# Kernel optimization log

Measured on AMD Instinct MI355X. Metric: run time of the kernel, lower is better.

## Reference

```python
import jax, jax.numpy as jnp
import numpy as np

BLOCK = 32      # block_size
KB = 128        # K // BLOCK (mask rows)
NB = 128        # N // BLOCK (mask cols)
DENSITY = 0.1


def _make_mask_indices():
    rng = np.random.RandomState(0)
    mask = rng.rand(KB, NB) < DENSITY
    # guarantee no fully-empty output column (kernel writes zeros there anyway,
    # segment_sum also yields zeros, so this is only to keep stats sane)
    ii, jj = np.nonzero(mask)   # row-major order == torch.nonzero(mask)
    return ii.astype(np.int32), jj.astype(np.int32)


def setup_inputs() -> dict:
    key = jax.random.key(0)
    k1, k2 = jax.random.split(key)
    ii, jj = _make_mask_indices()
    nnz = ii.shape[0]
    M = 4096
    K = KB * BLOCK
    x = jax.random.normal(k1, (M, K), dtype=jnp.float32)
    # block-sparse weight: one [BLOCK, BLOCK] tile per nonzero mask entry,
    # stored in row-major nonzero order (matches torch.nonzero ordering)
    w = jax.random.normal(k2, (nnz, BLOCK, BLOCK), dtype=jnp.float32) * 0.02
    return {"x": x, "w": w, "idx_i": jnp.asarray(ii), "idx_j": jnp.asarray(jj)}


def reference(x, w, idx_i, idx_j):
    # y[:, j*B:(j+1)*B] += x[:, i*B:(i+1)*B] @ w[blk] for each nonzero block (i, j)
    M, K = x.shape
    nnz, B, _ = w.shape
    xb = x.reshape(M, K // B, B)[:, idx_i, :]                 # [M, nnz, B] gather
    partial = jnp.einsum('mnk,nkj->nmj', xb, w)               # [nnz, M, B]
    yb = jax.ops.segment_sum(partial, idx_j, num_segments=NB)  # [NB, M, B] scatter-add
    return yb.transpose(1, 0, 2).reshape(M, NB * B)           # [M, N]
```

## Files before the change

kernel.cpp:

```cpp
#include <hip/hip_runtime.h>
#include <hip/hip_bf16.h>

typedef __bf16 bf16x8 __attribute__((ext_vector_type(8)));
typedef __bf16 bf16x4 __attribute__((ext_vector_type(4)));
typedef float f32x4 __attribute__((ext_vector_type(4)));

#define KDIM 4096
#define NDIM 4096
#define NBJ  128
#define KB   128

#define NB      7
#define BLK_LDS 2560

__global__ __launch_bounds__(256) void k_prep(
    const float* __restrict__ x, const float* __restrict__ w,
    const int* __restrict__ idx_i, const int* __restrict__ idx_j,
    __bf16* __restrict__ xb, __bf16* __restrict__ wT,
    int* __restrict__ colptr, int* __restrict__ colinfo,
    int nnz, int M, int nbCvt) {
    __shared__ char smem[2176];
    int b = blockIdx.x, t = threadIdx.x;

    if (b < nbCvt) {
        int i, m0;
        if ((M & 1023) == 0) {
            int cpx = M >> 9;
            int s = b & 7, r = b >> 3;
            int wch = r >> 7;
            i  = r & (KB - 1);
            m0 = (s * cpx + wch) * 64;
        } else {
            i  = b & (KB - 1);
            m0 = (b >> 7) * 64;
        }
        int q  = t & 3, r = t >> 2;
        const float* xp = x + (size_t)(m0 + r) * KDIM + i * 32 + q * 8;
        float4 u = ((const float4*)xp)[0];
        float4 v = ((const float4*)xp)[1];
        bf16x8 o;
        o[0]=(__bf16)u.x; o[1]=(__bf16)u.y; o[2]=(__bf16)u.z; o[3]=(__bf16)u.w;
        o[4]=(__bf16)v.x; o[5]=(__bf16)v.y; o[6]=(__bf16)v.z; o[7]=(__bf16)v.w;
        *(bf16x8*)(xb + ((size_t)i * M + m0 + r) * 32 + q * 8) = o;
    } else if (b < nbCvt + nnz) {
        auto tile = (__bf16(*)[33])smem;
        int n = b - nbCvt;
        float4 v = ((const float4*)(w + (size_t)n * 1024))[t];
        int e = t * 4, k = e >> 5, c = e & 31;
        tile[k][c + 0] = (__bf16)v.x; tile[k][c + 1] = (__bf16)v.y;
        tile[k][c + 2] = (__bf16)v.z; tile[k][c + 3] = (__bf16)v.w;
        __syncthreads();
        int f = t * 4, cc = f >> 5, kk = f & 31;
        bf16x4 o;
        o[0] = tile[kk + 0][cc]; o[1] = tile[kk + 1][cc];
        o[2] = tile[kk + 2][cc]; o[3] = tile[kk + 3][cc];
        ((bf16x4*)(wT + (size_t)n * 1024))[t] = o;
    } else {
        int* cnt = (int*)smem;
        int* cur = cnt + NBJ;
        if (t < NBJ) cnt[t] = 0;
        __syncthreads();
        for (int n = t; n < nnz; n += 256) atomicAdd(&cnt[idx_j[n]], 1);
        __syncthreads();
        int mycount = (t < NBJ) ? cnt[t] : 0;
        for (int off = 1; off < NBJ; off <<= 1) {
            int add = (t < NBJ && t >= off) ? cnt[t - off] : 0;
            __syncthreads();
            if (t < NBJ) cnt[t] += add;
            __syncthreads();
        }
        if (t < NBJ) {
            colptr[t + 1] = cnt[t];
            cur[t] = cnt[t] - mycount;
            if (t == 0) colptr[0] = 0;
        }
        __syncthreads();
        for (int n = t; n < nnz; n += 256) {
            int j = idx_j[n];
            int pos = atomicAdd(&cur[j], 1);
            colinfo[pos] = (idx_i[n] << 16) | n;
        }
    }
}

struct AFrag { bf16x8 a0, a1; };

#define MFMA4(A, B0, B1)                                                       \
    acc[0][0] = __builtin_amdgcn_mfma_f32_16x16x32_bf16(A.a0, B0, acc[0][0], 0, 0, 0); \
    acc[0][1] = __builtin_amdgcn_mfma_f32_16x16x32_bf16(A.a0, B1, acc[0][1], 0, 0, 0); \
    acc[1][0] = __builtin_amdgcn_mfma_f32_16x16x32_bf16(A.a1, B0, acc[1][0], 0, 0, 0); \
    acc[1][1] = __builtin_amdgcn_mfma_f32_16x16x32_bf16(A.a1, B1, acc[1][1], 0, 0, 0);

__global__ __launch_bounds__(256, 8) void k_bsmm(
    const __bf16* __restrict__ xb, const __bf16* __restrict__ wT,
    const int* __restrict__ colptr, const int* __restrict__ colinfo,
    float* __restrict__ y, int M) {
    __shared__ int nfo[64];
    __shared__ __attribute__((aligned(16))) char wbuf[NB * BLK_LDS];

    int RCH = M >> 7;
    int l = blockIdx.x;
    int rc, j;
    if ((RCH & 7) == 0) {
        int rps = RCH >> 3;
        int s = l & 7, u = l >> 3;
        rc = s * rps + (u >> 7);
        j  = u & (NBJ - 1);
    } else {
        rc = l % RCH; j = l / RCH;
    }
    int t = threadIdx.x;
    int lane = t & 63, wave = t >> 6;
    int quad = lane >> 4, l16 = lane & 15;
    int wrow = rc * 128 + wave * 32;

    int beg = colptr[j], end = colptr[j + 1];
    int cnt = end - beg;

    f32x4 acc[2][2] = {};

    size_t strideA = (size_t)M * 32;
    const __bf16* xbase = xb + (size_t)(wrow + l16) * 32 + quad * 8;
    const char*   wread = wbuf + l16 * 80 + quad * 16;

    if (cnt > 0 && cnt <= 64) {
        if (t < cnt) nfo[t] = colinfo[beg + t];
        __syncthreads();

        for (int bb0 = 0; bb0 < cnt; bb0 += NB) {
            int cb = cnt - bb0; if (cb > NB) cb = NB;
            if (bb0 > 0) __syncthreads();

            for (int c = t; c < cb * 128; c += 256) {
                int b = c >> 7, w16 = c & 127;
                int n = nfo[bb0 + b] & 0xFFFF;
                bf16x8 v = *(const bf16x8*)(wT + (size_t)n * 1024 + w16 * 8);
                *(bf16x8*)(wbuf + b * BLK_LDS + (w16 >> 2) * 80 + (w16 & 3) * 16) = v;
            }
            __syncthreads();

            auto fa = [&](int p) {
                int pp = p < cb ? p : cb - 1;
                int ib = nfo[bb0 + pp] >> 16;
                AFrag f;
                const __bf16* xp = xbase + (size_t)ib * strideA;
                f.a0 = *(const bf16x8*)(xp);
                f.a1 = *(const bf16x8*)(xp + 16 * 32);
                return f;
            };
            AFrag A0 = fa(0);
            AFrag A1 = fa(1);
            for (int p = 0; p < cb; ++p) {
                const char* wp = wread + p * BLK_LDS;
                bf16x8 b0 = *(const bf16x8*)(wp);
                bf16x8 b1 = *(const bf16x8*)(wp + 16 * 80);
                MFMA4(A0, b0, b1);
                A0 = A1; A1 = fa(p + 2);
            }
        }
    } else if (cnt > 64) {
        for (int bb = beg; bb < end; bb += NB) {
            int cb = end - bb; if (cb > NB) cb = NB;
            if (bb > beg) __syncthreads();
            if (t < cb) nfo[t] = colinfo[bb + t];
            __syncthreads();
            for (int c = t; c < cb * 128; c += 256) {
                int b = c >> 7, w16 = c & 127;
                int n = nfo[b] & 0xFFFF;
                bf16x8 v = *(const bf16x8*)(wT + (size_t)n * 1024 + w16 * 8);
                *(bf16x8*)(wbuf + b * BLK_LDS + (w16 >> 2) * 80 + (w16 & 3) * 16) = v;
            }
            __syncthreads();
            auto fa = [&](int p) {
                int pp = p < cb ? p : cb - 1;
                int ib = nfo[pp] >> 16;
                AFrag f;
                const __bf16* xp = xbase + (size_t)ib * strideA;
                f.a0 = *(const bf16x8*)(xp);
                f.a1 = *(const bf16x8*)(xp + 16 * 32);
                return f;
            };
            AFrag A0 = fa(0);
            AFrag A1 = fa(1);
            for (int p = 0; p < cb; ++p) {
                const char* wp = wread + p * BLK_LDS;
                bf16x8 b0 = *(const bf16x8*)(wp);
                bf16x8 b1 = *(const bf16x8*)(wp + 16 * 80);
                MFMA4(A0, b0, b1);
                A0 = A1; A1 = fa(p + 2);
            }
        }
    }

    #pragma unroll
    for (int r = 0; r < 2; ++r)
        #pragma unroll
        for (int ch = 0; ch < 2; ++ch)
            #pragma unroll
            for (int reg = 0; reg < 4; ++reg) {
                int row = wrow + r * 16 + quad * 4 + reg;
                int col = j * 32 + ch * 16 + l16;
                __builtin_nontemporal_store(acc[r][ch][reg],
                                            &y[(size_t)row * NDIM + col]);
            }
}

__global__ __launch_bounds__(256) void k_bsmm_nows(
    const float* __restrict__ x, const float* __restrict__ w,
    const int* __restrict__ idx_i, const int* __restrict__ idx_j,
    float* __restrict__ y, int nnz) {
    __shared__ int list[256];
    __shared__ int listn;
    __shared__ __bf16 tw[32][40];
    int j = blockIdx.y;
    int tid = threadIdx.x;
    int lane = tid & 63, wave = tid >> 6;
    int quad = lane >> 4, l16 = lane & 15;
    int wrow = blockIdx.x * 256 + wave * 64;

    if (tid == 0) listn = 0;
    __syncthreads();
    for (int n = tid; n < nnz; n += 256)
        if (idx_j[n] == j) { int p = atomicAdd(&listn, 1); list[p & 255] = n; }
    __syncthreads();
    int cnt = listn;

    f32x4 acc[4][2] = {};
    for (int p = 0; p < cnt; ++p) {
        int n = list[p];
        int ib = idx_i[n];
        {
            float4 v = ((const float4*)(w + (size_t)n * 1024))[tid];
            int e = tid * 4, k = e >> 5, c = e & 31;
            tw[c + 0][k] = (__bf16)v.x; tw[c + 1][k] = (__bf16)v.y;
            tw[c + 2][k] = (__bf16)v.z; tw[c + 3][k] = (__bf16)v.w;
        }
        __syncthreads();
        bf16x8 a[4];
        #pragma unroll
        for (int r = 0; r < 4; ++r) {
            const float* xp = x + (size_t)(wrow + r * 16 + l16) * KDIM + ib * 32 + quad * 8;
            float4 u = *(const float4*)(xp);
            float4 v = *(const float4*)(xp + 4);
            a[r][0] = (__bf16)u.x; a[r][1] = (__bf16)u.y; a[r][2] = (__bf16)u.z; a[r][3] = (__bf16)u.w;
            a[r][4] = (__bf16)v.x; a[r][5] = (__bf16)v.y; a[r][6] = (__bf16)v.z; a[r][7] = (__bf16)v.w;
        }
        bf16x8 b0 = *(const bf16x8*)&tw[l16][quad * 8];
        bf16x8 b1 = *(const bf16x8*)&tw[l16 + 16][quad * 8];
        #pragma unroll
        for (int r = 0; r < 4; ++r) {
            acc[r][0] = __builtin_amdgcn_mfma_f32_16x16x32_bf16(a[r], b0, acc[r][0], 0, 0, 0);
            acc[r][1] = __builtin_amdgcn_mfma_f32_16x16x32_bf16(a[r], b1, acc[r][1], 0, 0, 0);
        }
        __syncthreads();
    }

    #pragma unroll
    for (int r = 0; r < 4; ++r)
        #pragma unroll
        for (int ch = 0; ch < 2; ++ch)
            #pragma unroll
            for (int reg = 0; reg < 4; ++reg) {
                int row = wrow + r * 16 + quad * 4 + reg;
                int col = j * 32 + ch * 16 + l16;
                y[(size_t)row * NDIM + col] = acc[r][ch][reg];
            }
}

extern "C" void kernel_launch(void* const* d_in, const int* in_sizes, int n_in,
                              void* d_out, int out_size, void* d_ws, size_t ws_size,
                              hipStream_t stream) {
    const float* x     = (const float*)d_in[0];
    const float* w     = (const float*)d_in[1];
    const int*   idx_i = (const int*)d_in[2];
    const int*   idx_j = (const int*)d_in[3];
    float*       y     = (float*)d_out;

    int nnz = in_sizes[2];
    int M   = in_sizes[0] / KDIM;

    size_t xb_bytes = (size_t)M * KDIM * 2;
    size_t wt_bytes = (size_t)nnz * 1024 * 2;
    size_t need = xb_bytes + wt_bytes + (size_t)(NBJ + 2 + nnz) * 4;

    if (ws_size >= need && (M & 255) == 0 && nnz < 65536) {
        __bf16* xb      = (__bf16*)d_ws;
        __bf16* wT      = (__bf16*)((char*)d_ws + xb_bytes);
        int*    colptr  = (int*)((char*)d_ws + xb_bytes + wt_bytes);
        int*    colinfo = colptr + NBJ + 1;
        int nbCvt = KB * (M / 64);
        k_prep<<<nbCvt + nnz + 1, 256, 0, stream>>>(x, w, idx_i, idx_j,
                                                    xb, wT, colptr, colinfo,
                                                    nnz, M, nbCvt);
        k_bsmm<<<(M / 128) * NBJ, 256, 0, stream>>>(xb, wT, colptr, colinfo, y, M);
    } else {
        k_bsmm_nows<<<dim3(M / 256, NBJ), 256, 0, stream>>>(x, w, idx_i, idx_j, y, nnz);
    }
}
```

Before: 171.3 us.

## Stage A and W tiles into LDS via direct global-to-LDS loads

Replaces register-prefetched global reads of the x slab and the register-staged copy of weight tiles with global_load_lds transfers that write both A and B tiles directly into LDS, then feeds the MFMAs from LDS. The batch size drops to 6 blocks, LDS use grows to about 60 KB per workgroup, and the occupancy hint in launch bounds is removed. Nontemporal output stores become plain stores. The aim is to cut VGPR staging and global-load latency in the inner loop. The cost is much lower occupancy from the larger LDS footprint, no overlap between loading and compute within a batch, and possible LDS bank conflicts from the unpadded 64-byte row stride.

```diff
diff --git a/kernel.cpp b/kernel.cpp
--- a/kernel.cpp
+++ b/kernel.cpp
@@ -10,8 +10,15 @@
 #define NBJ  128
 #define KB   128
 
-#define NB      7
-#define BLK_LDS 2560
+#define NB    6
+#define A_BLK 8192
+#define B_BLK 2048
+
+__device__ __forceinline__ void gload16(const void* g, void* l) {
+    __builtin_amdgcn_global_load_lds(
+        (const __attribute__((address_space(1))) void*)g,
+        (__attribute__((address_space(3))) void*)l, 16, 0, 0);
+}
 
 __global__ __launch_bounds__(256) void k_prep(
     const float* __restrict__ x, const float* __restrict__ w,
@@ -83,20 +90,19 @@
     }
 }
 
-struct AFrag { bf16x8 a0, a1; };
-
-#define MFMA4(A, B0, B1)                                                       \
-    acc[0][0] = __builtin_amdgcn_mfma_f32_16x16x32_bf16(A.a0, B0, acc[0][0], 0, 0, 0); \
-    acc[0][1] = __builtin_amdgcn_mfma_f32_16x16x32_bf16(A.a0, B1, acc[0][1], 0, 0, 0); \
-    acc[1][0] = __builtin_amdgcn_mfma_f32_16x16x32_bf16(A.a1, B0, acc[1][0], 0, 0, 0); \
-    acc[1][1] = __builtin_amdgcn_mfma_f32_16x16x32_bf16(A.a1, B1, acc[1][1], 0, 0, 0);
-
-__global__ __launch_bounds__(256, 8) void k_bsmm(
+#define MFMA4(A0, A1, B0, B1)                                                  \
+    acc[0][0] = __builtin_amdgcn_mfma_f32_16x16x32_bf16(A0, B0, acc[0][0], 0, 0, 0); \
+    acc[0][1] = __builtin_amdgcn_mfma_f32_16x16x32_bf16(A0, B1, acc[0][1], 0, 0, 0); \
+    acc[1][0] = __builtin_amdgcn_mfma_f32_16x16x32_bf16(A1, B0, acc[1][0], 0, 0, 0); \
+    acc[1][1] = __builtin_amdgcn_mfma_f32_16x16x32_bf16(A1, B1, acc[1][1], 0, 0, 0);
+
+__global__ __launch_bounds__(256) void k_bsmm(
     const __bf16* __restrict__ xb, const __bf16* __restrict__ wT,
     const int* __restrict__ colptr, const int* __restrict__ colinfo,
     float* __restrict__ y, int M) {
     __shared__ int nfo[64];
-    __shared__ __attribute__((aligned(16))) char wbuf[NB * BLK_LDS];
+    __shared__ __attribute__((aligned(16))) char abuf[NB * A_BLK];
+    __shared__ __attribute__((aligned(16))) char bbuf[NB * B_BLK];
 
     int RCH = M >> 7;
     int l = blockIdx.x;
@@ -120,8 +126,9 @@
     f32x4 acc[2][2] = {};
 
     size_t strideA = (size_t)M * 32;
-    const __bf16* xbase = xb + (size_t)(wrow + l16) * 32 + quad * 8;
-    const char*   wread = wbuf + l16 * 80 + quad * 16;
+    const __bf16* xslab = xb + (size_t)(rc * 128) * 32;
+    const int aoff0 = (wave * 32 + l16) * 64 + quad * 16;
+    const int boff0 = l16 * 64 + quad * 16;
 
     if (cnt > 0 && cnt <= 64) {
         if (t < cnt) nfo[t] = colinfo[beg + t];
@@ -131,31 +138,28 @@
             int cb = cnt - bb0; if (cb > NB) cb = NB;
             if (bb0 > 0) __syncthreads();
 
+            for (int c = t; c < cb * 512; c += 256) {
+                int b = c >> 9, off = c & 511;
+                int ib = nfo[bb0 + b] >> 16;
+                gload16(xslab + (size_t)ib * strideA + off * 8,
+                        abuf + b * A_BLK + off * 16);
+            }
             for (int c = t; c < cb * 128; c += 256) {
-                int b = c >> 7, w16 = c & 127;
+                int b = c >> 7, off = c & 127;
                 int n = nfo[bb0 + b] & 0xFFFF;
-                bf16x8 v = *(const bf16x8*)(wT + (size_t)n * 1024 + w16 * 8);
-                *(bf16x8*)(wbuf + b * BLK_LDS + (w16 >> 2) * 80 + (w16 & 3) * 16) = v;
-            }
-            __syncthreads();
-
-            auto fa = [&](int p) {
-                int pp = p < cb ? p : cb - 1;
-                int ib = nfo[bb0 + pp] >> 16;
-                AFrag f;
-                const __bf16* xp = xbase + (size_t)ib * strideA;
-                f.a0 = *(const bf16x8*)(xp);
-                f.a1 = *(const bf16x8*)(xp + 16 * 32);
-                return f;
-            };
-            AFrag A0 = fa(0);
-            AFrag A1 = fa(1);
+                gload16(wT + (size_t)n * 1024 + off * 8,
+                        bbuf + b * B_BLK + off * 16);
+            }
+            __syncthreads();
+
             for (int p = 0; p < cb; ++p) {
-                const char* wp = wread + p * BLK_LDS;
-                bf16x8 b0 = *(const bf16x8*)(wp);
-                bf16x8 b1 = *(const bf16x8*)(wp + 16 * 80);
-                MFMA4(A0, b0, b1);
-                A0 = A1; A1 = fa(p + 2);
+                const char* ap = abuf + p * A_BLK + aoff0;
+                const char* bp = bbuf + p * B_BLK + boff0;
+                bf16x8 a0 = *(const bf16x8*)(ap);
+                bf16x8 a1 = *(const bf16x8*)(ap + 16 * 64);
+                bf16x8 b0 = *(const bf16x8*)(bp);
+                bf16x8 b1 = *(const bf16x8*)(bp + 16 * 64);
+                MFMA4(a0, a1, b0, b1);
             }
         }
     } else if (cnt > 64) {
@@ -164,30 +168,27 @@
             if (bb > beg) __syncthreads();
             if (t < cb) nfo[t] = colinfo[bb + t];
             __syncthreads();
+            for (int c = t; c < cb * 512; c += 256) {
+                int b = c >> 9, off = c & 511;
+                int ib = nfo[b] >> 16;
+                gload16(xslab + (size_t)ib * strideA + off * 8,
+                        abuf + b * A_BLK + off * 16);
+            }
             for (int c = t; c < cb * 128; c += 256) {
-                int b = c >> 7, w16 = c & 127;
+                int b = c >> 7, off = c & 127;
                 int n = nfo[b] & 0xFFFF;
-                bf16x8 v = *(const bf16x8*)(wT + (size_t)n * 1024 + w16 * 8);
-                *(bf16x8*)(wbuf + b * BLK_LDS + (w16 >> 2) * 80 + (w16 & 3) * 16) = v;
-            }
-            __syncthreads();
-            auto fa = [&](int p) {
-                int pp = p < cb ? p : cb - 1;
-                int ib = nfo[pp] >> 16;
-                AFrag f;
-                const __bf16* xp = xbase + (size_t)ib * strideA;
-                f.a0 = *(const bf16x8*)(xp);
-                f.a1 = *(const bf16x8*)(xp + 16 * 32);
-                return f;
-            };
-            AFrag A0 = fa(0);
-            AFrag A1 = fa(1);
+                gload16(wT + (size_t)n * 1024 + off * 8,
+                        bbuf + b * B_BLK + off * 16);
+            }
+            __syncthreads();
             for (int p = 0; p < cb; ++p) {
-                const char* wp = wread + p * BLK_LDS;
-                bf16x8 b0 = *(const bf16x8*)(wp);
-                bf16x8 b1 = *(const bf16x8*)(wp + 16 * 80);
-                MFMA4(A0, b0, b1);
-                A0 = A1; A1 = fa(p + 2);
+                const char* ap = abuf + p * A_BLK + aoff0;
+                const char* bp = bbuf + p * B_BLK + boff0;
+                bf16x8 a0 = *(const bf16x8*)(ap);
+                bf16x8 a1 = *(const bf16x8*)(ap + 16 * 64);
+                bf16x8 b0 = *(const bf16x8*)(bp);
+                bf16x8 b1 = *(const bf16x8*)(bp + 16 * 64);
+                MFMA4(a0, a1, b0, b1);
             }
         }
     }
@@ -200,8 +201,7 @@
             for (int reg = 0; reg < 4; ++reg) {
                 int row = wrow + r * 16 + quad * 4 + reg;
                 int col = j * 32 + ch * 16 + l16;
-                __builtin_nontemporal_store(acc[r][ch][reg],
-                                            &y[(size_t)row * NDIM + col]);
+                y[(size_t)row * NDIM + col] = acc[r][ch][reg];
             }
 }
 
```

Measured after the change: 182.4 us. +6.5%, slower.

## Fuse x fp32-to-bf16 conversion into the block-sparse matmul loads

Applied to the files above, without the earlier changes.

Removes the separate prep pass that converted all of x to a bf16 workspace copy. The matmul kernel now gathers fp32 rows of x directly and converts them to bf16 in registers before the MFMA. This saves the full conversion read/write pass and its workspace. In exchange, the repeated gathers of x move twice the bytes, since each column block rereads x in fp32. Occupancy hint lowered and output stores switched from nontemporal to regular.

```diff
diff --git a/kernel.cpp b/kernel.cpp
--- a/kernel.cpp
+++ b/kernel.cpp
@@ -14,37 +14,17 @@
 #define BLK_LDS 2560
 
 __global__ __launch_bounds__(256) void k_prep(
-    const float* __restrict__ x, const float* __restrict__ w,
+    const float* __restrict__ w,
     const int* __restrict__ idx_i, const int* __restrict__ idx_j,
-    __bf16* __restrict__ xb, __bf16* __restrict__ wT,
+    __bf16* __restrict__ wT,
     int* __restrict__ colptr, int* __restrict__ colinfo,
-    int nnz, int M, int nbCvt) {
+    int nnz) {
     __shared__ char smem[2176];
     int b = blockIdx.x, t = threadIdx.x;
 
-    if (b < nbCvt) {
-        int i, m0;
-        if ((M & 1023) == 0) {
-            int cpx = M >> 9;
-            int s = b & 7, r = b >> 3;
-            int wch = r >> 7;
-            i  = r & (KB - 1);
-            m0 = (s * cpx + wch) * 64;
-        } else {
-            i  = b & (KB - 1);
-            m0 = (b >> 7) * 64;
-        }
-        int q  = t & 3, r = t >> 2;
-        const float* xp = x + (size_t)(m0 + r) * KDIM + i * 32 + q * 8;
-        float4 u = ((const float4*)xp)[0];
-        float4 v = ((const float4*)xp)[1];
-        bf16x8 o;
-        o[0]=(__bf16)u.x; o[1]=(__bf16)u.y; o[2]=(__bf16)u.z; o[3]=(__bf16)u.w;
-        o[4]=(__bf16)v.x; o[5]=(__bf16)v.y; o[6]=(__bf16)v.z; o[7]=(__bf16)v.w;
-        *(bf16x8*)(xb + ((size_t)i * M + m0 + r) * 32 + q * 8) = o;
-    } else if (b < nbCvt + nnz) {
+    if (b < nnz) {
         auto tile = (__bf16(*)[33])smem;
-        int n = b - nbCvt;
+        int n = b;
         float4 v = ((const float4*)(w + (size_t)n * 1024))[t];
         int e = t * 4, k = e >> 5, c = e & 31;
         tile[k][c + 0] = (__bf16)v.x; tile[k][c + 1] = (__bf16)v.y;
@@ -83,16 +63,23 @@
     }
 }
 
-struct AFrag { bf16x8 a0, a1; };
-
-#define MFMA4(A, B0, B1)                                                       \
-    acc[0][0] = __builtin_amdgcn_mfma_f32_16x16x32_bf16(A.a0, B0, acc[0][0], 0, 0, 0); \
-    acc[0][1] = __builtin_amdgcn_mfma_f32_16x16x32_bf16(A.a0, B1, acc[0][1], 0, 0, 0); \
-    acc[1][0] = __builtin_amdgcn_mfma_f32_16x16x32_bf16(A.a1, B0, acc[1][0], 0, 0, 0); \
-    acc[1][1] = __builtin_amdgcn_mfma_f32_16x16x32_bf16(A.a1, B1, acc[1][1], 0, 0, 0);
-
-__global__ __launch_bounds__(256, 8) void k_bsmm(
-    const __bf16* __restrict__ xb, const __bf16* __restrict__ wT,
+struct FStage { float4 u0, v0, u1, v1; };
+
+__device__ __forceinline__ bf16x8 cvt8(float4 u, float4 v) {
+    bf16x8 o;
+    o[0]=(__bf16)u.x; o[1]=(__bf16)u.y; o[2]=(__bf16)u.z; o[3]=(__bf16)u.w;
+    o[4]=(__bf16)v.x; o[5]=(__bf16)v.y; o[6]=(__bf16)v.z; o[7]=(__bf16)v.w;
+    return o;
+}
+
+#define MFMA4(A0, A1, B0, B1)                                                  \
+    acc[0][0] = __builtin_amdgcn_mfma_f32_16x16x32_bf16(A0, B0, acc[0][0], 0, 0, 0); \
+    acc[0][1] = __builtin_amdgcn_mfma_f32_16x16x32_bf16(A0, B1, acc[0][1], 0, 0, 0); \
+    acc[1][0] = __builtin_amdgcn_mfma_f32_16x16x32_bf16(A1, B0, acc[1][0], 0, 0, 0); \
+    acc[1][1] = __builtin_amdgcn_mfma_f32_16x16x32_bf16(A1, B1, acc[1][1], 0, 0, 0);
+
+__global__ __launch_bounds__(256, 6) void k_bsmm(
+    const float* __restrict__ x, const __bf16* __restrict__ wT,
     const int* __restrict__ colptr, const int* __restrict__ colinfo,
     float* __restrict__ y, int M) {
     __shared__ int nfo[64];
@@ -119,9 +106,9 @@
 
     f32x4 acc[2][2] = {};
 
-    size_t strideA = (size_t)M * 32;
-    const __bf16* xbase = xb + (size_t)(wrow + l16) * 32 + quad * 8;
-    const char*   wread = wbuf + l16 * 80 + quad * 16;
+    const float* xr0 = x + (size_t)(wrow + l16) * KDIM + quad * 8;
+    const float* xr1 = xr0 + (size_t)16 * KDIM;
+    const char*  wread = wbuf + l16 * 80 + quad * 16;
 
     if (cnt > 0 && cnt <= 64) {
         if (t < cnt) nfo[t] = colinfo[beg + t];
@@ -139,23 +126,26 @@
             }
             __syncthreads();
 
-            auto fa = [&](int p) {
+            auto fF = [&](int p) {
                 int pp = p < cb ? p : cb - 1;
                 int ib = nfo[bb0 + pp] >> 16;
-                AFrag f;
-                const __bf16* xp = xbase + (size_t)ib * strideA;
-                f.a0 = *(const bf16x8*)(xp);
-                f.a1 = *(const bf16x8*)(xp + 16 * 32);
-                return f;
+                const float* p0 = xr0 + ib * 32;
+                const float* p1 = xr1 + ib * 32;
+                FStage s;
+                s.u0 = ((const float4*)p0)[0]; s.v0 = ((const float4*)p0)[1];
+                s.u1 = ((const float4*)p1)[0]; s.v1 = ((const float4*)p1)[1];
+                return s;
             };
-            AFrag A0 = fa(0);
-            AFrag A1 = fa(1);
+            FStage F0 = fF(0);
+            FStage F1 = fF(1);
             for (int p = 0; p < cb; ++p) {
+                bf16x8 a0 = cvt8(F0.u0, F0.v0);
+                bf16x8 a1 = cvt8(F0.u1, F0.v1);
                 const char* wp = wread + p * BLK_LDS;
                 bf16x8 b0 = *(const bf16x8*)(wp);
                 bf16x8 b1 = *(const bf16x8*)(wp + 16 * 80);
-                MFMA4(A0, b0, b1);
-                A0 = A1; A1 = fa(p + 2);
+                MFMA4(a0, a1, b0, b1);
+                F0 = F1; F1 = fF(p + 2);
             }
         }
     } else if (cnt > 64) {
@@ -171,23 +161,26 @@
                 *(bf16x8*)(wbuf + b * BLK_LDS + (w16 >> 2) * 80 + (w16 & 3) * 16) = v;
             }
             __syncthreads();
-            auto fa = [&](int p) {
+            auto fF = [&](int p) {
                 int pp = p < cb ? p : cb - 1;
                 int ib = nfo[pp] >> 16;
-                AFrag f;
-                const __bf16* xp = xbase + (size_t)ib * strideA;
-                f.a0 = *(const bf16x8*)(xp);
-                f.a1 = *(const bf16x8*)(xp + 16 * 32);
-                return f;
+                const float* p0 = xr0 + ib * 32;
+                const float* p1 = xr1 + ib * 32;
+                FStage s;
+                s.u0 = ((const float4*)p0)[0]; s.v0 = ((const float4*)p0)[1];
+                s.u1 = ((const float4*)p1)[0]; s.v1 = ((const float4*)p1)[1];
+                return s;
             };
-            AFrag A0 = fa(0);
-            AFrag A1 = fa(1);
+            FStage F0 = fF(0);
+            FStage F1 = fF(1);
             for (int p = 0; p < cb; ++p) {
+                bf16x8 a0 = cvt8(F0.u0, F0.v0);
+                bf16x8 a1 = cvt8(F0.u1, F0.v1);
                 const char* wp = wread + p * BLK_LDS;
                 bf16x8 b0 = *(const bf16x8*)(wp);
                 bf16x8 b1 = *(const bf16x8*)(wp + 16 * 80);
-                MFMA4(A0, b0, b1);
-                A0 = A1; A1 = fa(p + 2);
+                MFMA4(a0, a1, b0, b1);
+                F0 = F1; F1 = fF(p + 2);
             }
         }
     }
@@ -200,8 +193,7 @@
             for (int reg = 0; reg < 4; ++reg) {
                 int row = wrow + r * 16 + quad * 4 + reg;
                 int col = j * 32 + ch * 16 + l16;
-                __builtin_nontemporal_store(acc[r][ch][reg],
-                                            &y[(size_t)row * NDIM + col]);
+                y[(size_t)row * NDIM + col] = acc[r][ch][reg];
             }
 }
 
@@ -279,20 +271,16 @@
     int nnz = in_sizes[2];
     int M   = in_sizes[0] / KDIM;
 
-    size_t xb_bytes = (size_t)M * KDIM * 2;
     size_t wt_bytes = (size_t)nnz * 1024 * 2;
-    size_t need = xb_bytes + wt_bytes + (size_t)(NBJ + 2 + nnz) * 4;
+    size_t need = wt_bytes + (size_t)(NBJ + 2 + nnz) * 4;
 
     if (ws_size >= need && (M & 255) == 0 && nnz < 65536) {
-        __bf16* xb      = (__bf16*)d_ws;
-        __bf16* wT      = (__bf16*)((char*)d_ws + xb_bytes);
-        int*    colptr  = (int*)((char*)d_ws + xb_bytes + wt_bytes);
+        __bf16* wT      = (__bf16*)d_ws;
+        int*    colptr  = (int*)((char*)d_ws + wt_bytes);
         int*    colinfo = colptr + NBJ + 1;
-        int nbCvt = KB * (M / 64);
-        k_prep<<<nbCvt + nnz + 1, 256, 0, stream>>>(x, w, idx_i, idx_j,
-                                                    xb, wT, colptr, colinfo,
-                                                    nnz, M, nbCvt);
-        k_bsmm<<<(M / 128) * NBJ, 256, 0, stream>>>(xb, wT, colptr, colinfo, y, M);
+        k_prep<<<nnz + 1, 256, 0, stream>>>(w, idx_i, idx_j,
+                                            wT, colptr, colinfo, nnz);
+        k_bsmm<<<(M / 128) * NBJ, 256, 0, stream>>>(x, wT, colptr, colinfo, y, M);
     } else {
         k_bsmm_nows<<<dim3(M / 256, NBJ), 256, 0, stream>>>(x, w, idx_i, idx_j, y, nnz);
     }
```

Result: slower. 230.4 us (+34.5%).
